# Performance work log

Measured on AMD Instinct MI355X. Metric: run time of the kernel, lower is better.

## Reference

```python
import jax, jax.numpy as jnp
import numpy as np


def _dequantize(qweight, scale, zero_point, bits, group_size):
    """Unpack int32-packed weights and apply group-wise dequantization.

    qweight:    [N, K // (32//bits)] int32, value i within an int32 at shift i*bits
    scale/zp:   [N, K // group_size]
    returns W:  [N, K] float32
    """
    vpi = 32 // bits  # values per int32
    mask = (1 << bits) - 1
    N, packed = qweight.shape
    K = packed * vpi
    shifts = (jnp.arange(vpi, dtype=jnp.int32) * bits)  # [vpi]
    # [N, packed, vpi] -> flatten so value i of each int32 lands at consecutive K positions
    q = (qweight[:, :, None] >> shifts[None, None, :]) & mask
    q = q.reshape(N, K // group_size, group_size).astype(jnp.float32)
    w = scale[:, :, None] * (q - zero_point[:, :, None])  # group-wise dequant
    return w.reshape(N, K)


def setup_inputs() -> dict:
    key = jax.random.key(0)
    k1, k2, k3, k4, k5 = jax.random.split(key, 5)
    B, S, K, N = 4, 2048, 4096, 4096
    bits, group_size = 4, 128
    vpi = 32 // bits
    num_groups = K // group_size
    x = jax.random.normal(k1, (B, S, K), dtype=jnp.float32)
    qweight = jax.random.randint(k2, (N, K // vpi), jnp.iinfo(jnp.int32).min,
                                 jnp.iinfo(jnp.int32).max, dtype=jnp.int32)
    scale = jax.random.uniform(k3, (N, num_groups), dtype=jnp.float32,
                               minval=0.001, maxval=0.02)
    zero_point = jax.random.uniform(k4, (N, num_groups), dtype=jnp.float32,
                                    minval=0.0, maxval=float((1 << bits) - 1))
    bias = jax.random.normal(k5, (N,), dtype=jnp.float32)
    return {"x": x, "qweight": qweight, "scale": scale, "zero_point": zero_point,
            "bias": bias, "bits": bits, "group_size": group_size}


def reference(x, qweight, scale, zero_point, bias, bits, group_size):
    # Fused dequant + GEMM: y = x @ W^T + b, W dequantized from packed int4 groups
    w = _dequantize(qweight, scale, zero_point, bits, group_size)  # [N, K]
    y = jnp.einsum('bsk,nk->bsn', x, w)
    return y + bias
```

## Files before the change

### kernel.cpp

```cpp
#include <hip/hip_runtime.h>

#define KD 4096
#define ND 4096
#define GRP 32
#define NT (KD / 64)

typedef unsigned short u16;
typedef float   f32x4  __attribute__((ext_vector_type(4)));
typedef __bf16  bf16x8 __attribute__((ext_vector_type(8)));
typedef unsigned short u16x8 __attribute__((ext_vector_type(8)));
typedef unsigned short u16x4 __attribute__((ext_vector_type(4)));

__device__ __forceinline__ u16 f2bf(float f) {
  unsigned u = __float_as_uint(f);
  return (u16)((u + 0x7fffu + ((u >> 16) & 1u)) >> 16);
}

__device__ __forceinline__ void async16(const void* g, void* l) {
  __builtin_amdgcn_global_load_lds(
      (const __attribute__((address_space(1))) unsigned int*)g,
      (__attribute__((address_space(3))) unsigned int*)l, 16, 0, 0);
}

__global__ __launch_bounds__(256) void prep_kernel(
    const int* __restrict__ qw, const float* __restrict__ scale,
    const float* __restrict__ zp, u16* __restrict__ wout,
    const float4* __restrict__ x, u16x4* __restrict__ xb, int nx) {
  const int nth = gridDim.x * 256;
  const int t0 = blockIdx.x * 256 + threadIdx.x;
  for (int idx4 = t0; idx4 < ND * (KD / 32); idx4 += nth) {
    int n = idx4 >> 7;
    int p4 = idx4 & 127;
    int g = p4 >> 2;
    float s = scale[n * GRP + g];
    float bz = -s * zp[n * GRP + g];
    int4 q4 = ((const int4*)qw)[idx4];
    const unsigned qv[4] = {(unsigned)q4.x, (unsigned)q4.y,
                            (unsigned)q4.z, (unsigned)q4.w};
#pragma unroll
    for (int k = 0; k < 4; ++k) {
      u16x8 hv;
#pragma unroll
      for (int i = 0; i < 8; ++i)
        hv[i] = f2bf(fmaf((float)((qv[k] >> (4 * i)) & 15u), s, bz));
      *(u16x8*)(wout + (size_t)idx4 * 32 + k * 8) = hv;
    }
  }
  for (int i = t0; i < nx; i += nth) {
    float4 v = x[i];
    u16x4 h;
    h[0] = f2bf(v.x); h[1] = f2bf(v.y); h[2] = f2bf(v.z); h[3] = f2bf(v.w);
    xb[i] = h;
  }
}

__global__ __launch_bounds__(512, 2) void gemm256(
    const u16* __restrict__ xb, const u16* __restrict__ wb,
    const float* __restrict__ bias, float* __restrict__ out) {
  __shared__ u16 As[2][256 * 64];
  __shared__ u16 Bs[2][256 * 64];
  const int tid = threadIdx.x;
  const int l = tid & 63, w = tid >> 6;
  const int wr = w >> 2, wc = w & 3;
  const int col = l & 15, quad = l >> 4, rsw = col & 7;
  const int lr = l >> 3, csrc = (l & 7) ^ lr;

  const int id = blockIdx.y * gridDim.x + blockIdx.x;
  const int nwg = gridDim.x * gridDim.y;
  const int q = nwg >> 3, r = nwg & 7;
  const int xcd = id & 7, off = id >> 3;
  const int wgid = (xcd < r ? xcd * (q + 1) : r * (q + 1) + (xcd - r) * q) + off;
  const int nb = gridDim.x;
  const int m0 = (wgid / nb) * 256;
  const int n0 = (wgid % nb) * 256;

  const u16* asrc = xb + (size_t)(m0 + w * 16 + lr) * KD + csrc * 8;
  const u16* bsrc = wb + (size_t)(n0 + w * 16 + lr) * KD + csrc * 8;

#define STAGE_A(t, h)                                                      \
  do {                                                                     \
    const u16* _g = asrc + (size_t)((h) * 128) * KD + (t) * 64;            \
    u16* _l = &As[(t) & 1][((h) * 128 + w * 16) * 64];                     \
    async16(_g, _l);                                                       \
    async16(_g + (size_t)8 * KD, _l + 8 * 64);                             \
  } while (0)
#define STAGE_B(t, h)                                                      \
  do {                                                                     \
    const u16* _g = bsrc + (size_t)((h) * 128) * KD + (t) * 64;            \
    u16* _l = &Bs[(t) & 1][((h) * 128 + w * 16) * 64];                     \
    async16(_g, _l);                                                       \
    async16(_g + (size_t)8 * KD, _l + 8 * 64);                             \
  } while (0)
#define BAR()   __builtin_amdgcn_s_barrier()
#define SB0()   __builtin_amdgcn_sched_barrier(0)
#define LGKM0() do { asm volatile("s_waitcnt lgkmcnt(0)"); SB0(); } while (0)
#define LDA(Ab, i, kk) \
  (*(const bf16x8*)&(Ab)[(wr * 128 + (i) * 16 + col) * 64 + ((((kk) * 4 + quad) ^ rsw) * 8)])
#define LDB(Bb, j, kk) \
  (*(const bf16x8*)&(Bb)[(wc * 64 + (j) * 16 + col) * 64 + ((((kk) * 4 + quad) ^ rsw) * 8)])
#define MFMA_BLK(IO, JO)                                                   \
  _Pragma("unroll")                                                        \
  for (int kk = 0; kk < 2; ++kk)                                           \
    _Pragma("unroll")                                                      \
    for (int i = 0; i < 4; ++i)                                            \
      _Pragma("unroll")                                                    \
      for (int j = 0; j < 2; ++j)                                          \
        acc[(IO) + i][(JO) + j] = __builtin_amdgcn_mfma_f32_16x16x32_bf16( \
            a[i][kk], b[(JO) + j][kk], acc[(IO) + i][(JO) + j], 0, 0, 0);
#define TILE(Ab, Bb, SB_STMT, SA_STMT, WAIT_STMT)                          \
  do {                                                                     \
    _Pragma("unroll")                                                      \
    for (int i = 0; i < 4; ++i) { a[i][0] = LDA(Ab, i, 0); a[i][1] = LDA(Ab, i, 1); } \
    _Pragma("unroll")                                                      \
    for (int j = 0; j < 2; ++j) { b[j][0] = LDB(Bb, j, 0); b[j][1] = LDB(Bb, j, 1); } \
    BAR(); LGKM0();                                                        \
    __builtin_amdgcn_s_setprio(1); MFMA_BLK(0, 0);                         \
    __builtin_amdgcn_s_setprio(0); BAR();                                  \
    _Pragma("unroll")                                                      \
    for (int j = 2; j < 4; ++j) { b[j][0] = LDB(Bb, j, 0); b[j][1] = LDB(Bb, j, 1); } \
    BAR(); LGKM0();                                                        \
    __builtin_amdgcn_s_setprio(1); MFMA_BLK(0, 2);                         \
    __builtin_amdgcn_s_setprio(0); BAR();                                  \
    _Pragma("unroll")                                                      \
    for (int i = 0; i < 4; ++i) { a[i][0] = LDA(Ab, i + 4, 0); a[i][1] = LDA(Ab, i + 4, 1); } \
    SB_STMT;                                                               \
    BAR(); LGKM0();                                                        \
    __builtin_amdgcn_s_setprio(1); MFMA_BLK(4, 0);                         \
    __builtin_amdgcn_s_setprio(0); BAR();                                  \
    SA_STMT;                                                               \
    __builtin_amdgcn_s_setprio(1); MFMA_BLK(4, 2);                         \
    __builtin_amdgcn_s_setprio(0);                                         \
    WAIT_STMT; SB0(); BAR();                                               \
  } while (0)

  f32x4 acc[8][4] = {};
  bf16x8 a[4][2], b[4][2];

  STAGE_B(0, 0); STAGE_B(0, 1); STAGE_A(0, 0); STAGE_A(0, 1);
  STAGE_B(1, 0); STAGE_B(1, 1); STAGE_A(1, 0); STAGE_A(1, 1);
  asm volatile("s_waitcnt vmcnt(8)");
  SB0();
  BAR();

  for (int tt = 0; tt < NT - 4; tt += 2) {
    TILE(As[0], Bs[0],
         { STAGE_B(tt + 2, 0); STAGE_B(tt + 2, 1); },
         { STAGE_A(tt + 2, 0); STAGE_A(tt + 2, 1); },
         asm volatile("s_waitcnt vmcnt(8)"));
    TILE(As[1], Bs[1],
         { STAGE_B(tt + 3, 0); STAGE_B(tt + 3, 1); },
         { STAGE_A(tt + 3, 0); STAGE_A(tt + 3, 1); },
         asm volatile("s_waitcnt vmcnt(8)"));
  }
  TILE(As[0], Bs[0],
       { STAGE_B(NT - 2, 0); STAGE_B(NT - 2, 1); },
       { STAGE_A(NT - 2, 0); STAGE_A(NT - 2, 1); },
       asm volatile("s_waitcnt vmcnt(8)"));
  TILE(As[1], Bs[1],
       { STAGE_B(NT - 1, 0); STAGE_B(NT - 1, 1); },
       { STAGE_A(NT - 1, 0); STAGE_A(NT - 1, 1); },
       asm volatile("s_waitcnt vmcnt(8)"));
  TILE(As[0], Bs[0], {;}, {;}, asm volatile("s_waitcnt vmcnt(0)"));
  TILE(As[1], Bs[1], {;}, {;}, ;);

#pragma unroll
  for (int j = 0; j < 4; ++j) {
    int n = n0 + wc * 64 + j * 16 + col;
    float bj = bias[n];
#pragma unroll
    for (int i = 0; i < 8; ++i) {
      int mrow = m0 + wr * 128 + i * 16 + quad * 4;
#pragma unroll
      for (int rr = 0; rr < 4; ++rr)
        out[(size_t)(mrow + rr) * ND + n] = acc[i][j][rr] + bj;
    }
  }
#undef STAGE_A
#undef STAGE_B
#undef BAR
#undef SB0
#undef LGKM0
#undef LDA
#undef LDB
#undef MFMA_BLK
#undef TILE
}

template <int XF32, int WQ>
__global__ __launch_bounds__(256, 3) void gemm_kernel(
    const u16*   __restrict__ xbp,
    const float* __restrict__ xf,
    const u16*   __restrict__ wbp,
    const int*   __restrict__ qw,
    const float* __restrict__ scale,
    const float* __restrict__ zp,
    const float* __restrict__ bias,
    float* __restrict__ out) {
  __shared__ u16 As[128 * 64];
  __shared__ u16 Bs[128 * 64];
  const int tid = threadIdx.x;
  const int l = tid & 63, w = tid >> 6;
  const int m0 = blockIdx.y * 128, n0 = blockIdx.x * 128;
  const int wm = (w >> 1) * 64, wn = (w & 1) * 64;
  const int col = l & 15, quad = l >> 4;
  const int rsw = col & 7;
  const int lr = l >> 3;
  const int csrc = (l & 7) ^ lr;
  f32x4 acc[4][4] = {};

  for (int k0 = 0; k0 < KD; k0 += 64) {
    __syncthreads();

    if constexpr (XF32) {
#pragma unroll
      for (int it = 0; it < 8; ++it) {
        int fi = it * 256 + tid;
        int row = fi >> 4, cs = fi & 15;
        float4 v = *(const float4*)(xf + (size_t)(m0 + row) * KD + k0 + cs * 4);
        u16x4 h;
        h[0] = f2bf(v.x); h[1] = f2bf(v.y); h[2] = f2bf(v.z); h[3] = f2bf(v.w);
        int slot = (cs >> 1) ^ (row & 7);
        *(u16x4*)(&As[row * 64 + slot * 8 + (cs & 1) * 4]) = h;
      }
    } else {
#pragma unroll
      for (int c = 0; c < 4; ++c) {
        int br = w * 32 + c * 8;
        const u16* g = xbp + (size_t)(m0 + br + lr) * KD + k0 + csrc * 8;
        async16(g, &As[br * 64]);
      }
    }

    if constexpr (WQ) {
#pragma unroll
      for (int it = 0; it < 4; ++it) {
        int qi = it * 256 + tid;
        int row = qi >> 3, p8 = qi & 7;
        int nrow = n0 + row;
        int g = k0 >> 7;
        float s = scale[nrow * GRP + g];
        float bz = -s * zp[nrow * GRP + g];
        unsigned qv = (unsigned)qw[(size_t)nrow * (KD / 8) + (k0 >> 3) + p8];
        u16x8 hv;
#pragma unroll
        for (int i = 0; i < 8; ++i)
          hv[i] = f2bf(fmaf((float)((qv >> (4 * i)) & 15u), s, bz));
        *(u16x8*)(&Bs[row * 64 + ((p8 ^ (row & 7)) * 8)]) = hv;
      }
    } else {
#pragma unroll
      for (int c = 0; c < 4; ++c) {
        int br = w * 32 + c * 8;
        const u16* g = wbp + (size_t)(n0 + br + lr) * KD + k0 + csrc * 8;
        async16(g, &Bs[br * 64]);
      }
    }

    __syncthreads();

#pragma unroll
    for (int kk = 0; kk < 2; ++kk) {
      bf16x8 a[4], b[4];
      const int slot = ((kk * 4 + quad) ^ rsw) * 8;
#pragma unroll
      for (int i = 0; i < 4; ++i)
        a[i] = *(const bf16x8*)&As[(wm + i * 16 + col) * 64 + slot];
#pragma unroll
      for (int j = 0; j < 4; ++j)
        b[j] = *(const bf16x8*)&Bs[(wn + j * 16 + col) * 64 + slot];
#pragma unroll
      for (int i = 0; i < 4; ++i)
#pragma unroll
        for (int j = 0; j < 4; ++j)
          acc[i][j] = __builtin_amdgcn_mfma_f32_16x16x32_bf16(a[i], b[j], acc[i][j], 0, 0, 0);
    }
  }

#pragma unroll
  for (int j = 0; j < 4; ++j) {
    int n = n0 + wn + j * 16 + col;
    float bj = bias[n];
#pragma unroll
    for (int i = 0; i < 4; ++i) {
      int mrow = m0 + wm + i * 16 + quad * 4;
#pragma unroll
      for (int rr = 0; rr < 4; ++rr)
        out[(size_t)(mrow + rr) * ND + n] = acc[i][j][rr] + bj;
    }
  }
}

extern "C" void kernel_launch(void* const* d_in, const int* in_sizes, int n_in,
                              void* d_out, int out_size, void* d_ws, size_t ws_size,
                              hipStream_t stream) {
  const float* x     = (const float*)d_in[0];
  const int*   qw    = (const int*)d_in[1];
  const float* scale = (const float*)d_in[2];
  const float* zp    = (const float*)d_in[3];
  const float* bias  = (const float*)d_in[4];
  float* out = (float*)d_out;

  const int M = in_sizes[0] / KD;

  const size_t needW = (size_t)ND * KD * sizeof(u16);
  const size_t needX = (size_t)M * KD * sizeof(u16);

  if (ws_size >= needW + needX && (M % 256) == 0) {
    u16* wb = (u16*)d_ws;
    u16* xbuf = wb + (size_t)ND * KD;
    prep_kernel<<<2048, 256, 0, stream>>>(qw, scale, zp, wb,
                                          (const float4*)x, (u16x4*)xbuf,
                                          M * (KD / 4));
    dim3 grid(ND / 256, M / 256);
    gemm256<<<grid, dim3(512), 0, stream>>>(xbuf, wb, bias, out);
  } else if (ws_size >= needW) {
    u16* wb = (u16*)d_ws;
    prep_kernel<<<2048, 256, 0, stream>>>(qw, scale, zp, wb, nullptr, nullptr, 0);
    dim3 grid(ND / 128, M / 128);
    gemm_kernel<1, 0><<<grid, dim3(256), 0, stream>>>(nullptr, x, wb, qw, scale, zp, bias, out);
  } else {
    dim3 grid(ND / 128, M / 128);
    gemm_kernel<1, 1><<<grid, dim3(256), 0, stream>>>(nullptr, x, nullptr, qw, scale, zp, bias, out);
  }
}
```

Baseline: 477.7 us.

## Simplify GEMM main loop to one-tile-ahead prefetch with full drain per tile

```diff
diff --git a/kernel.cpp b/kernel.cpp
--- a/kernel.cpp
+++ b/kernel.cpp
@@ -91,77 +91,61 @@
     async16(_g, _l);                                                       \
     async16(_g + (size_t)8 * KD, _l + 8 * 64);                             \
   } while (0)
+#define STAGE4(t) do { STAGE_B(t, 0); STAGE_B(t, 1); STAGE_A(t, 0); STAGE_A(t, 1); } while (0)
 #define BAR()   __builtin_amdgcn_s_barrier()
 #define SB0()   __builtin_amdgcn_sched_barrier(0)
-#define LGKM0() do { asm volatile("s_waitcnt lgkmcnt(0)"); SB0(); } while (0)
 #define LDA(Ab, i, kk) \
   (*(const bf16x8*)&(Ab)[(wr * 128 + (i) * 16 + col) * 64 + ((((kk) * 4 + quad) ^ rsw) * 8)])
 #define LDB(Bb, j, kk) \
   (*(const bf16x8*)&(Bb)[(wc * 64 + (j) * 16 + col) * 64 + ((((kk) * 4 + quad) ^ rsw) * 8)])
-#define MFMA_BLK(IO, JO)                                                   \
-  _Pragma("unroll")                                                        \
-  for (int kk = 0; kk < 2; ++kk)                                           \
-    _Pragma("unroll")                                                      \
-    for (int i = 0; i < 4; ++i)                                            \
+#define COMPUTE(Ab, Bb)                                                    \
+  do {                                                                     \
+    _Pragma("unroll")                                                      \
+    for (int i = 0; i < 4; ++i) { a[i][0] = LDA(Ab, i, 0); a[i][1] = LDA(Ab, i, 1); } \
+    _Pragma("unroll")                                                      \
+    for (int j = 0; j < 4; ++j) { b[j][0] = LDB(Bb, j, 0); b[j][1] = LDB(Bb, j, 1); } \
+    _Pragma("unroll")                                                      \
+    for (int kk = 0; kk < 2; ++kk)                                         \
       _Pragma("unroll")                                                    \
-      for (int j = 0; j < 2; ++j)                                          \
-        acc[(IO) + i][(JO) + j] = __builtin_amdgcn_mfma_f32_16x16x32_bf16( \
-            a[i][kk], b[(JO) + j][kk], acc[(IO) + i][(JO) + j], 0, 0, 0);
-#define TILE(Ab, Bb, SB_STMT, SA_STMT, WAIT_STMT)                          \
-  do {                                                                     \
-    _Pragma("unroll")                                                      \
-    for (int i = 0; i < 4; ++i) { a[i][0] = LDA(Ab, i, 0); a[i][1] = LDA(Ab, i, 1); } \
-    _Pragma("unroll")                                                      \
-    for (int j = 0; j < 2; ++j) { b[j][0] = LDB(Bb, j, 0); b[j][1] = LDB(Bb, j, 1); } \
-    BAR(); LGKM0();                                                        \
-    __builtin_amdgcn_s_setprio(1); MFMA_BLK(0, 0);                         \
-    __builtin_amdgcn_s_setprio(0); BAR();                                  \
-    _Pragma("unroll")                                                      \
-    for (int j = 2; j < 4; ++j) { b[j][0] = LDB(Bb, j, 0); b[j][1] = LDB(Bb, j, 1); } \
-    BAR(); LGKM0();                                                        \
-    __builtin_amdgcn_s_setprio(1); MFMA_BLK(0, 2);                         \
-    __builtin_amdgcn_s_setprio(0); BAR();                                  \
+      for (int i = 0; i < 4; ++i)                                          \
+        _Pragma("unroll")                                                  \
+        for (int j = 0; j < 4; ++j)                                        \
+          acc[i][j] = __builtin_amdgcn_mfma_f32_16x16x32_bf16(             \
+              a[i][kk], b[j][kk], acc[i][j], 0, 0, 0);                     \
     _Pragma("unroll")                                                      \
     for (int i = 0; i < 4; ++i) { a[i][0] = LDA(Ab, i + 4, 0); a[i][1] = LDA(Ab, i + 4, 1); } \
-    SB_STMT;                                                               \
-    BAR(); LGKM0();                                                        \
-    __builtin_amdgcn_s_setprio(1); MFMA_BLK(4, 0);                         \
-    __builtin_amdgcn_s_setprio(0); BAR();                                  \
-    SA_STMT;                                                               \
-    __builtin_amdgcn_s_setprio(1); MFMA_BLK(4, 2);                         \
-    __builtin_amdgcn_s_setprio(0);                                         \
-    WAIT_STMT; SB0(); BAR();                                               \
+    _Pragma("unroll")                                                      \
+    for (int kk = 0; kk < 2; ++kk)                                         \
+      _Pragma("unroll")                                                    \
+      for (int i = 0; i < 4; ++i)                                          \
+        _Pragma("unroll")                                                  \
+        for (int j = 0; j < 4; ++j)                                        \
+          acc[4 + i][j] = __builtin_amdgcn_mfma_f32_16x16x32_bf16(         \
+              a[i][kk], b[j][kk], acc[4 + i][j], 0, 0, 0);                 \
   } while (0)
+#define DRAIN() do { asm volatile("s_waitcnt vmcnt(0)"); SB0(); BAR(); } while (0)
 
   f32x4 acc[8][4] = {};
   bf16x8 a[4][2], b[4][2];
 
-  STAGE_B(0, 0); STAGE_B(0, 1); STAGE_A(0, 0); STAGE_A(0, 1);
-  STAGE_B(1, 0); STAGE_B(1, 1); STAGE_A(1, 0); STAGE_A(1, 1);
-  asm volatile("s_waitcnt vmcnt(8)");
+  STAGE4(0);
+  DRAIN();
+
+  for (int tt = 0; tt < NT - 2; tt += 2) {
+    STAGE4(tt + 1);
+    SB0();
+    COMPUTE(As[0], Bs[0]);
+    DRAIN();
+    STAGE4(tt + 2);
+    SB0();
+    COMPUTE(As[1], Bs[1]);
+    DRAIN();
+  }
+  STAGE4(NT - 1);
   SB0();
-  BAR();
-
-  for (int tt = 0; tt < NT - 4; tt += 2) {
-    TILE(As[0], Bs[0],
-         { STAGE_B(tt + 2, 0); STAGE_B(tt + 2, 1); },
-         { STAGE_A(tt + 2, 0); STAGE_A(tt + 2, 1); },
-         asm volatile("s_waitcnt vmcnt(8)"));
-    TILE(As[1], Bs[1],
-         { STAGE_B(tt + 3, 0); STAGE_B(tt + 3, 1); },
-         { STAGE_A(tt + 3, 0); STAGE_A(tt + 3, 1); },
-         asm volatile("s_waitcnt vmcnt(8)"));
-  }
-  TILE(As[0], Bs[0],
-       { STAGE_B(NT - 2, 0); STAGE_B(NT - 2, 1); },
-       { STAGE_A(NT - 2, 0); STAGE_A(NT - 2, 1); },
-       asm volatile("s_waitcnt vmcnt(8)"));
-  TILE(As[1], Bs[1],
-       { STAGE_B(NT - 1, 0); STAGE_B(NT - 1, 1); },
-       { STAGE_A(NT - 1, 0); STAGE_A(NT - 1, 1); },
-       asm volatile("s_waitcnt vmcnt(8)"));
-  TILE(As[0], Bs[0], {;}, {;}, asm volatile("s_waitcnt vmcnt(0)"));
-  TILE(As[1], Bs[1], {;}, {;}, ;);
+  COMPUTE(As[0], Bs[0]);
+  DRAIN();
+  COMPUTE(As[1], Bs[1]);
 
 #pragma unroll
   for (int j = 0; j < 4; ++j) {
@@ -177,13 +161,13 @@
   }
 #undef STAGE_A
 #undef STAGE_B
+#undef STAGE4
 #undef BAR
 #undef SB0
-#undef LGKM0
 #undef LDA
 #undef LDB
-#undef MFMA_BLK
-#undef TILE
+#undef COMPUTE
+#undef DRAIN
 }
 
 template <int XF32, int WQ>
```

Measured after the change: 480.1 us. No clear change (+0.5%).
